# Kernel tuning notes

Hardware: AMD Instinct MI355X
Metric: run time of the kernel (lower is better)

## Reference

```python
import jax, jax.numpy as jnp
import numpy as np

NS = 100000   # served nodes
NI = 100000   # interfered nodes
E = 1000000   # edges per relation
D = 64        # 2 * Nt_num, Nt_num = 32
HM = 32       # message MLP hidden
HU = 16       # update MLP hidden


def _lin_init(key, fan_in, fan_out):
    s = 1.0 / np.sqrt(fan_in)
    kw, kb = jax.random.split(key)
    w = jax.random.uniform(kw, (fan_in, fan_out), jnp.float32, -s, s)
    b = jax.random.uniform(kb, (fan_out,), jnp.float32, -s, s)
    return w, b


def setup_inputs() -> dict:
    key = jax.random.key(0)
    ks = jax.random.split(key, 12)
    wm1, bm1 = _lin_init(ks[0], D, HM)
    wm2, bm2 = _lin_init(ks[1], HM, D)
    wu1, bu1 = _lin_init(ks[2], D, HU)
    wu2, bu2 = _lin_init(ks[3], HU, D)
    wo, bo = _lin_init(ks[4], D, D)
    edge_s2i = jnp.stack([
        jax.random.randint(ks[5], (E,), 0, NS),   # src in served
        jax.random.randint(ks[6], (E,), 0, NI),   # dst in interfered
    ]).astype(jnp.int64)
    edge_i2s = jnp.stack([
        jax.random.randint(ks[7], (E,), 0, NI),   # src in interfered
        jax.random.randint(ks[8], (E,), 0, NS),   # dst in served
    ]).astype(jnp.int64)
    return {
        "x_served": jax.random.normal(ks[9], (NS, D), jnp.float32),
        "x_interfered": jax.random.normal(ks[10], (NI, D), jnp.float32),
        "edge_s2i": edge_s2i,
        "edge_i2s": edge_i2s,
        "wm1": wm1, "bm1": bm1, "wm2": wm2, "bm2": bm2,
        "wu1": wu1, "bu1": bu1, "wu2": wu2, "bu2": bu2,
        "wo": wo, "bo": bo,
    }


def reference(x_served, x_interfered, edge_s2i, edge_i2s,
              wm1, bm1, wm2, bm2, wu1, bu1, wu2, bu2, wo, bo):
    def mlp_m(h):  # MLP([D, 32, D]): Lin+ReLU, Lin+ReLU
        return jax.nn.relu(jax.nn.relu(h @ wm1 + bm1) @ wm2 + bm2)

    def mlp_u(h):  # MLP([D, 16, D])
        return jax.nn.relu(jax.nn.relu(h @ wu1 + bu1) @ wu2 + bu2)

    def conv(x_src, edges, n_dst):
        # gather source node features per edge, per-edge message MLP
        msg = mlp_m(x_src[edges[0]])                    # [E, D]
        # scatter-sum into destination nodes
        agg = jax.ops.segment_sum(msg, edges[1], num_segments=n_dst)
        return mlp_u(agg)                               # [n_dst, D]

    xs, xi = x_served, x_interfered
    for _ in range(3):
        new_i = conv(xs, edge_s2i, NI)   # served -> interfered
        new_s = conv(xi, edge_i2s, NS)   # interfered -> served
        xs, xi = new_s, new_i
    # h2o on served: Lin + Tanh -> beamforming matrix
    return jnp.tanh(xs @ wo + bo)
```

## Files before the change

kernel.cpp:

```cpp
#include <hip/hip_runtime.h>
#include <hip/hip_fp16.h>
#include <math.h>

constexpr int D = 64;
constexpr int CAP = 48;
constexpr int RPB = 256;
constexpr int EPB = 4096;

typedef _Float16 half2_t __attribute__((ext_vector_type(2)));

__device__ inline float fdot2(unsigned a, unsigned b, float c){
    return __builtin_amdgcn_fdot2(__builtin_bit_cast(half2_t, a),
                                  __builtin_bit_cast(half2_t, b), c, false);
}

__device__ inline unsigned pack2(float lo, float hi){
    __half2 h = __floats2half2_rn(lo, hi);
    return *(unsigned*)&h;
}

__device__ inline void ld16u(const unsigned* base, unsigned* w){
    const uint4* p = (const uint4*)base;
    uint4 a = p[0], b = p[1], c = p[2], d = p[3];
    w[0]=a.x;  w[1]=a.y;  w[2]=a.z;  w[3]=a.w;
    w[4]=b.x;  w[5]=b.y;  w[6]=b.z;  w[7]=b.w;
    w[8]=c.x;  w[9]=c.y;  w[10]=c.z; w[11]=c.w;
    w[12]=d.x; w[13]=d.y; w[14]=d.z; w[15]=d.w;
}

__device__ inline void store_half8(__half* dst, const float* o){
    uint4 w;
    w.x = pack2(o[0], o[1]); w.y = pack2(o[2], o[3]);
    w.z = pack2(o[4], o[5]); w.w = pack2(o[6], o[7]);
    *((uint4*)dst) = w;
}

__device__ inline void load_half8(const __half* src, float* r){
    uint4 w = *((const uint4*)src);
    __half2* h = (__half2*)&w;
    float2 f0 = __half22float2(h[0]);
    float2 f1 = __half22float2(h[1]);
    float2 f2 = __half22float2(h[2]);
    float2 f3 = __half22float2(h[3]);
    r[0] = f0.x; r[1] = f0.y; r[2] = f1.x; r[3] = f1.y;
    r[4] = f2.x; r[5] = f2.y; r[6] = f3.x; r[7] = f3.y;
}


__global__ void __launch_bounds__(256) k_bucket_mlpm(
        const int* __restrict__ es2i, const int* __restrict__ ei2s, int E, int NI,
        int NBUK, int BSTRIDE,
        int* __restrict__ gcur, unsigned* __restrict__ buckets,
        const float* __restrict__ x,
        const float* __restrict__ wm1, const float* __restrict__ bm1,
        const float* __restrict__ wm2, const float* __restrict__ bm2,
        __half* __restrict__ y, int Nmlp, int nbEdge)
{
    __shared__ __align__(16) char smem[12544];
    int t = threadIdx.x;

    if ((int)blockIdx.x < nbEdge){
        int* hist = (int*)smem;
        int* base = (int*)(smem + 4096);
        int* offs = (int*)(smem + 8192);
        for (int i = t; i < NBUK; i += 256){ hist[i] = 0; offs[i] = 0; }
        __syncthreads();
        int e0 = blockIdx.x * EPB + t;
        int rr[16], ss[16];
        #pragma unroll
        for (int k = 0; k < 16; k++){
            int i = e0 + k*256;
            if (i < E){
                ss[k] = es2i[i];            rr[k] = es2i[E + i];
            } else if (i < 2*E){
                int j = i - E;
                ss[k] = ei2s[j];            rr[k] = NI + ei2s[E + j];
            } else rr[k] = -1;
        }
        #pragma unroll
        for (int k = 0; k < 16; k++)
            if (rr[k] >= 0) atomicAdd(&hist[rr[k] >> 8], 1);
        __syncthreads();
        for (int b = t; b < NBUK; b += 256){
            int h = hist[b];
            base[b] = h ? atomicAdd(&gcur[b], h) : 0;
        }
        __syncthreads();
        #pragma unroll
        for (int k = 0; k < 16; k++){
            if (rr[k] >= 0){
                int b = rr[k] >> 8;
                int p = base[b] + atomicAdd(&offs[b], 1);
                if (p < BSTRIDE)
                    buckets[(size_t)b*BSTRIDE + p] =
                        ((unsigned)(rr[k] & 255) << 24) | (unsigned)ss[k];
            }
        }
        return;
    }

    unsigned* w1p = (unsigned*)smem;
    unsigned* w2p = (unsigned*)(smem + 4096);
    float*    sb1 = (float*)(smem + 8192);
    float*    sb2 = (float*)(smem + 8320);
    for (int i = t; i < 1024; i += 256){ int kp=i>>5, j=i&31; w1p[i]=pack2(wm1[(2*kp)*32+j], wm1[(2*kp+1)*32+j]); }
    for (int i = t; i < 1024; i += 256){ int jp=i>>6, c=i&63; w2p[i]=pack2(wm2[(2*jp)*64+c], wm2[(2*jp+1)*64+c]); }
    if (t < 32) sb1[t] = bm1[t];
    if (t < 64) sb2[t] = bm2[t];
    __syncthreads();
    int n = ((int)blockIdx.x - nbEdge)*256 + t;
    if (n >= Nmlp) return;

    const float4* xp = (const float4*)(x + (size_t)n*D);
    unsigned xq[32];
    #pragma unroll
    for (int i = 0; i < 16; i++){
        float4 v = xp[i];
        xq[2*i]   = pack2(v.x, v.y);
        xq[2*i+1] = pack2(v.z, v.w);
    }
    float h[32];
    #pragma unroll
    for (int j = 0; j < 32; j++) h[j] = 0.f;
    #pragma unroll
    for (int kp = 0; kp < 32; kp++){
        unsigned xv = xq[kp];
        unsigned w[32];
        ld16u(&w1p[kp*32],      w);
        ld16u(&w1p[kp*32 + 16], w + 16);
        #pragma unroll
        for (int j = 0; j < 32; j++) h[j] = fdot2(xv, w[j], h[j]);
    }
    #pragma unroll
    for (int j = 0; j < 32; j++) h[j] = fmaxf(h[j] + sb1[j], 0.f);
    unsigned hh[16];
    #pragma unroll
    for (int jp = 0; jp < 16; jp++) hh[jp] = pack2(h[2*jp], h[2*jp+1]);

    __half* yrow = y + (size_t)n*D;
    #pragma unroll
    for (int c0 = 0; c0 < 64; c0 += 32){
        float o[32];
        #pragma unroll
        for (int c = 0; c < 32; c++) o[c] = sb2[c0 + c];
        #pragma unroll
        for (int jp = 0; jp < 16; jp++){
            unsigned hv = hh[jp];
            unsigned w[32];
            ld16u(&w2p[jp*64 + c0],      w);
            ld16u(&w2p[jp*64 + c0 + 16], w + 16);
            #pragma unroll
            for (int c = 0; c < 32; c++) o[c] = fdot2(hv, w[c], o[c]);
        }
        #pragma unroll
        for (int c = 0; c < 32; c++) o[c] = fmaxf(o[c], 0.f);
        store_half8(yrow + c0,      &o[0]);
        store_half8(yrow + c0 + 8,  &o[8]);
        store_half8(yrow + c0 + 16, &o[16]);
        store_half8(yrow + c0 + 24, &o[24]);
    }
}


__global__ void __launch_bounds__(512) k_scatter_lds(const int* __restrict__ gcur,
        const unsigned* __restrict__ buckets, int BSTRIDE, int NTOT,
        int* __restrict__ cnt, int* __restrict__ slots)
{
    __shared__ int lcnt[RPB];
    __shared__ int lslots[RPB*CAP];
    int t = threadIdx.x;
    int b = blockIdx.x;
    int r0 = b * RPB;
    int nrows = NTOT - r0; if (nrows > RPB) nrows = RPB;

    for (int i = t; i < RPB; i += 512) lcnt[i] = 0;
    __syncthreads();

    int n = gcur[b]; if (n > BSTRIDE) n = BSTRIDE;
    const unsigned* bp = buckets + (size_t)b*BSTRIDE;
    for (int k = t; k < n; k += 512){
        unsigned e = bp[k];
        int lr  = e >> 24;
        int src = e & 0xFFFFFF;
        int pos = atomicAdd(&lcnt[lr], 1);
        if (pos < CAP) lslots[lr*CAP + pos] = src;
    }
    __syncthreads();

    int4* gs = (int4*)(slots + (size_t)r0*CAP);
    const int4* ls = (const int4*)lslots;
    int n4 = nrows*CAP/4;
    for (int i = t; i < n4; i += 512) gs[i] = ls[i];
    for (int i = t; i < nrows; i += 512) cnt[r0 + i] = lcnt[i];
}


__global__ void __launch_bounds__(256) k_agg(const __half* __restrict__ M,
        const int* __restrict__ cnt, const int* __restrict__ slots,
        __half* __restrict__ agg, int N)
{
    int gid  = blockIdx.x*256 + threadIdx.x;
    int node = gid >> 6;
    if (node >= N) return;
    int lane = gid & 63;
    int sub  = lane >> 3;
    int fl   = lane & 7;
    int deg = cnt[node]; deg = deg < CAP ? deg : CAP;
    const int* row = slots + (size_t)node*CAP;
    float acc[8];
    #pragma unroll
    for (int i = 0; i < 8; i++) acc[i] = 0.f;
    for (int k = sub; k < deg; k += 8){
        int s = row[k];
        float v[8];
        load_half8(M + (size_t)s*D + fl*8, v);
        #pragma unroll
        for (int i = 0; i < 8; i++) acc[i] += v[i];
    }
    #pragma unroll
    for (int i = 0; i < 8; i++){
        acc[i] += __shfl_xor(acc[i], 8);
        acc[i] += __shfl_xor(acc[i], 16);
        acc[i] += __shfl_xor(acc[i], 32);
    }
    if (sub == 0) store_half8(agg + (size_t)node*D + fl*8, acc);
}


__global__ void __launch_bounds__(256) k_mlp_um(const __half* __restrict__ agg,
        const float* __restrict__ wu1, const float* __restrict__ bu1,
        const float* __restrict__ wu2, const float* __restrict__ bu2,
        const float* __restrict__ wm1, const float* __restrict__ bm1,
        const float* __restrict__ wm2, const float* __restrict__ bm2,
        __half* __restrict__ y, int N)
{
    __shared__ __align__(16) unsigned w1p[32*16];
    __shared__ __align__(16) unsigned w2p[8*64];
    __shared__ __align__(16) unsigned m1p[32*32];
    __shared__ __align__(16) unsigned m2p[16*64];
    __shared__ float sbu1[16], sbu2[64], sbm1[32], sbm2[64];
    int t = threadIdx.x;
    for (int i = t; i < 512;  i += 256){ int kp=i>>4, j=i&15; w1p[i]=pack2(wu1[(2*kp)*16+j], wu1[(2*kp+1)*16+j]); }
    for (int i = t; i < 512;  i += 256){ int jp=i>>6, c=i&63; w2p[i]=pack2(wu2[(2*jp)*64+c], wu2[(2*jp+1)*64+c]); }
    for (int i = t; i < 1024; i += 256){ int kp=i>>5, j=i&31; m1p[i]=pack2(wm1[(2*kp)*32+j], wm1[(2*kp+1)*32+j]); }
    for (int i = t; i < 1024; i += 256){ int kp=i>>6, c=i&63; m2p[i]=pack2(wm2[(2*kp)*64+c], wm2[(2*kp+1)*64+c]); }
    if (t < 16) sbu1[t] = bu1[t];
    if (t < 64) sbu2[t] = bu2[t];
    if (t < 32) sbm1[t] = bm1[t];
    if (t < 64) sbm2[t] = bm2[t];
    __syncthreads();
    int n = blockIdx.x*256 + t;
    if (n >= N) return;

    unsigned xq[32];
    {
        const uint4* p = (const uint4*)(agg + (size_t)n*D);
        #pragma unroll
        for (int i = 0; i < 8; i++){
            uint4 w = p[i];
            xq[4*i] = w.x; xq[4*i+1] = w.y; xq[4*i+2] = w.z; xq[4*i+3] = w.w;
        }
    }

    float h[16];
    #pragma unroll
    for (int j = 0; j < 16; j++) h[j] = 0.f;
    #pragma unroll
    for (int kp = 0; kp < 32; kp++){
        unsigned a = xq[kp];
        unsigned w[16];
        ld16u(&w1p[kp*16], w);
        #pragma unroll
        for (int j = 0; j < 16; j++) h[j] = fdot2(a, w[j], h[j]);
    }
    #pragma unroll
    for (int j = 0; j < 16; j++) h[j] = fmaxf(h[j] + sbu1[j], 0.f);
    unsigned hp[8];
    #pragma unroll
    for (int jp = 0; jp < 8; jp++) hp[jp] = pack2(h[2*jp], h[2*jp+1]);

    #pragma unroll
    for (int c0 = 0; c0 < 64; c0 += 32){
        float o[32];
        #pragma unroll
        for (int c = 0; c < 32; c++) o[c] = sbu2[c0 + c];
        #pragma unroll
        for (int jp = 0; jp < 8; jp++){
            unsigned a = hp[jp];
            unsigned w[32];
            ld16u(&w2p[jp*64 + c0],      w);
            ld16u(&w2p[jp*64 + c0 + 16], w + 16);
            #pragma unroll
            for (int c = 0; c < 32; c++) o[c] = fdot2(a, w[c], o[c]);
        }
        #pragma unroll
        for (int c = 0; c < 32; c += 2)
            xq[(c0 + c) >> 1] = pack2(fmaxf(o[c], 0.f), fmaxf(o[c+1], 0.f));
    }

    float hm[32];
    #pragma unroll
    for (int j = 0; j < 32; j++) hm[j] = 0.f;
    #pragma unroll
    for (int kp = 0; kp < 32; kp++){
        unsigned a = xq[kp];
        unsigned w[32];
        ld16u(&m1p[kp*32],      w);
        ld16u(&m1p[kp*32 + 16], w + 16);
        #pragma unroll
        for (int j = 0; j < 32; j++) hm[j] = fdot2(a, w[j], hm[j]);
    }
    #pragma unroll
    for (int j = 0; j < 32; j++) hm[j] = fmaxf(hm[j] + sbm1[j], 0.f);
    unsigned hq[16];
    #pragma unroll
    for (int jp = 0; jp < 16; jp++) hq[jp] = pack2(hm[2*jp], hm[2*jp+1]);

    __half* yrow = y + (size_t)n*D;
    #pragma unroll
    for (int c0 = 0; c0 < 64; c0 += 32){
        float o[32];
        #pragma unroll
        for (int c = 0; c < 32; c++) o[c] = sbm2[c0 + c];
        #pragma unroll
        for (int kp = 0; kp < 16; kp++){
            unsigned a = hq[kp];
            unsigned w[32];
            ld16u(&m2p[kp*64 + c0],      w);
            ld16u(&m2p[kp*64 + c0 + 16], w + 16);
            #pragma unroll
            for (int c = 0; c < 32; c++) o[c] = fdot2(a, w[c], o[c]);
        }
        #pragma unroll
        for (int c = 0; c < 32; c++) o[c] = fmaxf(o[c], 0.f);
        store_half8(yrow + c0,      &o[0]);
        store_half8(yrow + c0 + 8,  &o[8]);
        store_half8(yrow + c0 + 16, &o[16]);
        store_half8(yrow + c0 + 24, &o[24]);
    }
}


__device__ inline float fast_tanh(float x){
    float ax = fabsf(x);
    float e  = __expf(2.f*ax);
    float t  = 1.f - 2.f/(e + 1.f);
    return copysignf(t, x);
}

__global__ void __launch_bounds__(256) k_mlp_uo(const __half* __restrict__ agg,
        const float* __restrict__ wu1, const float* __restrict__ bu1,
        const float* __restrict__ wu2, const float* __restrict__ bu2,
        const float* __restrict__ wo,  const float* __restrict__ bo,
        float* __restrict__ out, int N)
{
    __shared__ __align__(16) unsigned w1p[32*16];
    __shared__ __align__(16) unsigned w2p[8*64];
    __shared__ __align__(16) unsigned wop[32*64];
    __shared__ float sbu1[16], sbu2[64], sbo[64];
    int t = threadIdx.x;
    for (int i = t; i < 512;  i += 256){ int kp=i>>4, j=i&15; w1p[i]=pack2(wu1[(2*kp)*16+j], wu1[(2*kp+1)*16+j]); }
    for (int i = t; i < 512;  i += 256){ int jp=i>>6, c=i&63; w2p[i]=pack2(wu2[(2*jp)*64+c], wu2[(2*jp+1)*64+c]); }
    for (int i = t; i < 2048; i += 256){ int kp=i>>6, c=i&63; wop[i]=pack2(wo[(2*kp)*64+c], wo[(2*kp+1)*64+c]); }
    if (t < 16) sbu1[t] = bu1[t];
    if (t < 64) sbu2[t] = bu2[t];
    if (t < 64) sbo[t]  = bo[t];
    __syncthreads();
    int n = blockIdx.x*256 + t;
    if (n >= N) return;

    unsigned xq[32];
    {
        const uint4* p = (const uint4*)(agg + (size_t)n*D);
        #pragma unroll
        for (int i = 0; i < 8; i++){
            uint4 w = p[i];
            xq[4*i] = w.x; xq[4*i+1] = w.y; xq[4*i+2] = w.z; xq[4*i+3] = w.w;
        }
    }

    float h[16];
    #pragma unroll
    for (int j = 0; j < 16; j++) h[j] = 0.f;
    #pragma unroll
    for (int kp = 0; kp < 32; kp++){
        unsigned a = xq[kp];
        unsigned w[16];
        ld16u(&w1p[kp*16], w);
        #pragma unroll
        for (int j = 0; j < 16; j++) h[j] = fdot2(a, w[j], h[j]);
    }
    #pragma unroll
    for (int j = 0; j < 16; j++) h[j] = fmaxf(h[j] + sbu1[j], 0.f);
    unsigned hp[8];
    #pragma unroll
    for (int jp = 0; jp < 8; jp++) hp[jp] = pack2(h[2*jp], h[2*jp+1]);

    #pragma unroll
    for (int c0 = 0; c0 < 64; c0 += 32){
        float o[32];
        #pragma unroll
        for (int c = 0; c < 32; c++) o[c] = sbu2[c0 + c];
        #pragma unroll
        for (int jp = 0; jp < 8; jp++){
            unsigned a = hp[jp];
            unsigned w[32];
            ld16u(&w2p[jp*64 + c0],      w);
            ld16u(&w2p[jp*64 + c0 + 16], w + 16);
            #pragma unroll
            for (int c = 0; c < 32; c++) o[c] = fdot2(a, w[c], o[c]);
        }
        #pragma unroll
        for (int c = 0; c < 32; c += 2)
            xq[(c0 + c) >> 1] = pack2(fmaxf(o[c], 0.f), fmaxf(o[c+1], 0.f));
    }

    float* orow = out + (size_t)n*D;
    #pragma unroll
    for (int c0 = 0; c0 < 64; c0 += 32){
        float o[32];
        #pragma unroll
        for (int c = 0; c < 32; c++) o[c] = sbo[c0 + c];
        #pragma unroll
        for (int kp = 0; kp < 32; kp++){
            unsigned a = xq[kp];
            unsigned w[32];
            ld16u(&wop[kp*64 + c0],      w);
            ld16u(&wop[kp*64 + c0 + 16], w + 16);
            #pragma unroll
            for (int c = 0; c < 32; c++) o[c] = fdot2(a, w[c], o[c]);
        }
        float4* op = (float4*)(orow + c0);
        #pragma unroll
        for (int i = 0; i < 8; i++){
            float4 v;
            v.x = fast_tanh(o[4*i]);
            v.y = fast_tanh(o[4*i+1]);
            v.z = fast_tanh(o[4*i+2]);
            v.w = fast_tanh(o[4*i+3]);
            op[i] = v;
        }
    }
}


extern "C" void kernel_launch(void* const* d_in, const int* in_sizes, int n_in,
                              void* d_out, int out_size, void* d_ws, size_t ws_size,
                              hipStream_t stream)
{
    const float* x_interfered = (const float*)d_in[1];
    const int*   e_s2i        = (const int*)d_in[2];
    const int*   e_i2s        = (const int*)d_in[3];
    const float* wm1 = (const float*)d_in[4];  const float* bm1 = (const float*)d_in[5];
    const float* wm2 = (const float*)d_in[6];  const float* bm2 = (const float*)d_in[7];
    const float* wu1 = (const float*)d_in[8];  const float* bu1 = (const float*)d_in[9];
    const float* wu2 = (const float*)d_in[10]; const float* bu2 = (const float*)d_in[11];
    const float* wo  = (const float*)d_in[12]; const float* bo  = (const float*)d_in[13];

    const int NS = in_sizes[0] / D;
    const int NI = in_sizes[1] / D;
    const int E  = in_sizes[2] / 2;
    const int NMAX = (NS > NI) ? NS : NI;
    const int NTOT = NI + NS;

    const int NBUK = ((NTOT - 1) >> 8) + 1;
    int avg = (2*E) / NBUK;
    const int BSTRIDE = ((2*avg) + 1023) & ~1023;

    char* p = (char*)d_ws;
    auto alloc = [&](size_t bytes) -> void* {
        void* r = (void*)p;
        p += (bytes + 255) & ~(size_t)255;
        return r;
    };
    __half*   M      = (__half*)alloc((size_t)NMAX*D*2);
    __half*   AGG    = (__half*)alloc((size_t)NMAX*D*2);
    int*      cnt    = (int*)alloc((size_t)NTOT*4);
    int*      gcur   = (int*)alloc((size_t)NBUK*4);
    int*      slots  = (int*)alloc((size_t)NTOT*CAP*4);
    unsigned* buckets= (unsigned*)alloc((size_t)NBUK*BSTRIDE*4);
    (void)ws_size; (void)n_in; (void)out_size;

    const int* cnt_i = cnt;
    const int* cnt_s = cnt + NI;
    const int* slots_i = slots;
    const int* slots_s = slots + (size_t)NI*CAP;

    hipMemsetAsync(gcur, 0, (size_t)NBUK*4, stream);

    const int nbEdge = (2*E + EPB - 1)/EPB;
    const int nbMlp  = (NI + 255)/256;
    k_bucket_mlpm<<<nbEdge + nbMlp, 256, 0, stream>>>(
        e_s2i, e_i2s, E, NI, NBUK, BSTRIDE, gcur, buckets,
        x_interfered, wm1, bm1, wm2, bm2, M, NI, nbEdge);
    k_scatter_lds<<<NBUK, 512, 0, stream>>>(gcur, buckets, BSTRIDE, NTOT, cnt, slots);

    k_agg<<<((size_t)NS*64 + 255)/256, 256, 0, stream>>>(M, cnt_s, slots_s, AGG, NS);
    k_mlp_um<<<(NS + 255)/256, 256, 0, stream>>>(AGG, wu1, bu1, wu2, bu2,
                                               wm1, bm1, wm2, bm2, M, NS);
    k_agg<<<((size_t)NI*64 + 255)/256, 256, 0, stream>>>(M, cnt_i, slots_i, AGG, NI);
    k_mlp_um<<<(NI + 255)/256, 256, 0, stream>>>(AGG, wu1, bu1, wu2, bu2,
                                               wm1, bm1, wm2, bm2, M, NI);
    k_agg<<<((size_t)NS*64 + 255)/256, 256, 0, stream>>>(M, cnt_s, slots_s, AGG, NS);
    k_mlp_uo<<<(NS + 255)/256, 256, 0, stream>>>(AGG, wu1, bu1, wu2, bu2,
                                               wo, bo, (float*)d_out, NS);
}
```

Before: 248.1 us.

## Process two nodes per thread in MLP kernels and halve edge-bucketing chunk

The node-MLP kernels now run 128 threads per block, and each thread handles two nodes. Every weight fragment read from shared memory is reused for both nodes, which cuts LDS traffic per FLOP, and output chunks shrink to 16 columns to limit register pressure. Separately, the edge-bucketing blocks each take 2048 edges instead of 4096. That doubles the block count for parallelism but also doubles the per-block histogram init and the global atomic traffic. The two-node register arrays may raise VGPR use and lower occupancy.

```diff
diff --git a/kernel.cpp b/kernel.cpp
--- a/kernel.cpp
+++ b/kernel.cpp
@@ -5,7 +5,7 @@
 constexpr int D = 64;
 constexpr int CAP = 48;
 constexpr int RPB = 256;
-constexpr int EPB = 4096;
+constexpr int EPB = 2048;
 
 typedef _Float16 half2_t __attribute__((ext_vector_type(2)));
 
@@ -66,9 +66,9 @@
         for (int i = t; i < NBUK; i += 256){ hist[i] = 0; offs[i] = 0; }
         __syncthreads();
         int e0 = blockIdx.x * EPB + t;
-        int rr[16], ss[16];
-        #pragma unroll
-        for (int k = 0; k < 16; k++){
+        int rr[8], ss[8];
+        #pragma unroll
+        for (int k = 0; k < 8; k++){
             int i = e0 + k*256;
             if (i < E){
                 ss[k] = es2i[i];            rr[k] = es2i[E + i];
@@ -78,7 +78,7 @@
             } else rr[k] = -1;
         }
         #pragma unroll
-        for (int k = 0; k < 16; k++)
+        for (int k = 0; k < 8; k++)
             if (rr[k] >= 0) atomicAdd(&hist[rr[k] >> 8], 1);
         __syncthreads();
         for (int b = t; b < NBUK; b += 256){
@@ -87,7 +87,7 @@
         }
         __syncthreads();
         #pragma unroll
-        for (int k = 0; k < 16; k++){
+        for (int k = 0; k < 8; k++){
             if (rr[k] >= 0){
                 int b = rr[k] >> 8;
                 int p = base[b] + atomicAdd(&offs[b], 1);
@@ -227,7 +227,7 @@
 }
 
 
-__global__ void __launch_bounds__(256) k_mlp_um(const __half* __restrict__ agg,
+__global__ void __launch_bounds__(128) k_mlp_um(const __half* __restrict__ agg,
         const float* __restrict__ wu1, const float* __restrict__ bu1,
         const float* __restrict__ wu2, const float* __restrict__ bu2,
         const float* __restrict__ wm1, const float* __restrict__ bm1,
@@ -240,103 +240,143 @@
     __shared__ __align__(16) unsigned m2p[16*64];
     __shared__ float sbu1[16], sbu2[64], sbm1[32], sbm2[64];
     int t = threadIdx.x;
-    for (int i = t; i < 512;  i += 256){ int kp=i>>4, j=i&15; w1p[i]=pack2(wu1[(2*kp)*16+j], wu1[(2*kp+1)*16+j]); }
-    for (int i = t; i < 512;  i += 256){ int jp=i>>6, c=i&63; w2p[i]=pack2(wu2[(2*jp)*64+c], wu2[(2*jp+1)*64+c]); }
-    for (int i = t; i < 1024; i += 256){ int kp=i>>5, j=i&31; m1p[i]=pack2(wm1[(2*kp)*32+j], wm1[(2*kp+1)*32+j]); }
-    for (int i = t; i < 1024; i += 256){ int kp=i>>6, c=i&63; m2p[i]=pack2(wm2[(2*kp)*64+c], wm2[(2*kp+1)*64+c]); }
+    for (int i = t; i < 512;  i += 128){ int kp=i>>4, j=i&15; w1p[i]=pack2(wu1[(2*kp)*16+j], wu1[(2*kp+1)*16+j]); }
+    for (int i = t; i < 512;  i += 128){ int jp=i>>6, c=i&63; w2p[i]=pack2(wu2[(2*jp)*64+c], wu2[(2*jp+1)*64+c]); }
+    for (int i = t; i < 1024; i += 128){ int kp=i>>5, j=i&31; m1p[i]=pack2(wm1[(2*kp)*32+j], wm1[(2*kp+1)*32+j]); }
+    for (int i = t; i < 1024; i += 128){ int kp=i>>6, c=i&63; m2p[i]=pack2(wm2[(2*kp)*64+c], wm2[(2*kp+1)*64+c]); }
     if (t < 16) sbu1[t] = bu1[t];
     if (t < 64) sbu2[t] = bu2[t];
     if (t < 32) sbm1[t] = bm1[t];
     if (t < 64) sbm2[t] = bm2[t];
     __syncthreads();
-    int n = blockIdx.x*256 + t;
-    if (n >= N) return;
-
-    unsigned xq[32];
+    int base = blockIdx.x*256;
+    int n0 = base + t;
+    int n1 = base + t + 128;
+    bool has0 = n0 < N;
+    bool has1 = n1 < N;
+    if (!has0) return;
+
+    unsigned xq0[32], xq1[32];
     {
-        const uint4* p = (const uint4*)(agg + (size_t)n*D);
+        const uint4* p = (const uint4*)(agg + (size_t)n0*D);
         #pragma unroll
         for (int i = 0; i < 8; i++){
             uint4 w = p[i];
-            xq[4*i] = w.x; xq[4*i+1] = w.y; xq[4*i+2] = w.z; xq[4*i+3] = w.w;
-        }
-    }
-
-    float h[16];
-    #pragma unroll
-    for (int j = 0; j < 16; j++) h[j] = 0.f;
+            xq0[4*i] = w.x; xq0[4*i+1] = w.y; xq0[4*i+2] = w.z; xq0[4*i+3] = w.w;
+        }
+    }
+    if (has1){
+        const uint4* p = (const uint4*)(agg + (size_t)n1*D);
+        #pragma unroll
+        for (int i = 0; i < 8; i++){
+            uint4 w = p[i];
+            xq1[4*i] = w.x; xq1[4*i+1] = w.y; xq1[4*i+2] = w.z; xq1[4*i+3] = w.w;
+        }
+    } else {
+        #pragma unroll
+        for (int i = 0; i < 32; i++) xq1[i] = 0u;
+    }
+
+    float h0[16], h1[16];
+    #pragma unroll
+    for (int j = 0; j < 16; j++){ h0[j] = 0.f; h1[j] = 0.f; }
     #pragma unroll
     for (int kp = 0; kp < 32; kp++){
-        unsigned a = xq[kp];
+        unsigned a0 = xq0[kp], a1 = xq1[kp];
         unsigned w[16];
         ld16u(&w1p[kp*16], w);
         #pragma unroll
-        for (int j = 0; j < 16; j++) h[j] = fdot2(a, w[j], h[j]);
-    }
-    #pragma unroll
-    for (int j = 0; j < 16; j++) h[j] = fmaxf(h[j] + sbu1[j], 0.f);
-    unsigned hp[8];
-    #pragma unroll
-    for (int jp = 0; jp < 8; jp++) hp[jp] = pack2(h[2*jp], h[2*jp+1]);
-
-    #pragma unroll
-    for (int c0 = 0; c0 < 64; c0 += 32){
-        float o[32];
-        #pragma unroll
-        for (int c = 0; c < 32; c++) o[c] = sbu2[c0 + c];
+        for (int j = 0; j < 16; j++){
+            h0[j] = fdot2(a0, w[j], h0[j]);
+            h1[j] = fdot2(a1, w[j], h1[j]);
+        }
+    }
+    unsigned hp0[8], hp1[8];
+    #pragma unroll
+    for (int jp = 0; jp < 8; jp++){
+        float a0 = fmaxf(h0[2*jp]   + sbu1[2*jp],   0.f);
+        float b0 = fmaxf(h0[2*jp+1] + sbu1[2*jp+1], 0.f);
+        float a1 = fmaxf(h1[2*jp]   + sbu1[2*jp],   0.f);
+        float b1 = fmaxf(h1[2*jp+1] + sbu1[2*jp+1], 0.f);
+        hp0[jp] = pack2(a0, b0);
+        hp1[jp] = pack2(a1, b1);
+    }
+
+    #pragma unroll
+    for (int c0 = 0; c0 < 64; c0 += 16){
+        float o0[16], o1[16];
+        #pragma unroll
+        for (int c = 0; c < 16; c++){ float bv = sbu2[c0 + c]; o0[c] = bv; o1[c] = bv; }
         #pragma unroll
         for (int jp = 0; jp < 8; jp++){
-            unsigned a = hp[jp];
-            unsigned w[32];
-            ld16u(&w2p[jp*64 + c0],      w);
-            ld16u(&w2p[jp*64 + c0 + 16], w + 16);
+            unsigned a0 = hp0[jp], a1 = hp1[jp];
+            unsigned w[16];
+            ld16u(&w2p[jp*64 + c0], w);
             #pragma unroll
-            for (int c = 0; c < 32; c++) o[c] = fdot2(a, w[c], o[c]);
-        }
-        #pragma unroll
-        for (int c = 0; c < 32; c += 2)
-            xq[(c0 + c) >> 1] = pack2(fmaxf(o[c], 0.f), fmaxf(o[c+1], 0.f));
-    }
-
-    float hm[32];
-    #pragma unroll
-    for (int j = 0; j < 32; j++) hm[j] = 0.f;
+            for (int c = 0; c < 16; c++){
+                o0[c] = fdot2(a0, w[c], o0[c]);
+                o1[c] = fdot2(a1, w[c], o1[c]);
+            }
+        }
+        #pragma unroll
+        for (int c = 0; c < 16; c += 2){
+            xq0[(c0 + c) >> 1] = pack2(fmaxf(o0[c], 0.f), fmaxf(o0[c+1], 0.f));
+            xq1[(c0 + c) >> 1] = pack2(fmaxf(o1[c], 0.f), fmaxf(o1[c+1], 0.f));
+        }
+    }
+
+    float hm0[32], hm1[32];
+    #pragma unroll
+    for (int j = 0; j < 32; j++){ hm0[j] = 0.f; hm1[j] = 0.f; }
     #pragma unroll
     for (int kp = 0; kp < 32; kp++){
-        unsigned a = xq[kp];
+        unsigned a0 = xq0[kp], a1 = xq1[kp];
         unsigned w[32];
         ld16u(&m1p[kp*32],      w);
         ld16u(&m1p[kp*32 + 16], w + 16);
         #pragma unroll
-        for (int j = 0; j < 32; j++) hm[j] = fdot2(a, w[j], hm[j]);
-    }
-    #pragma unroll
-    for (int j = 0; j < 32; j++) hm[j] = fmaxf(hm[j] + sbm1[j], 0.f);
-    unsigned hq[16];
-    #pragma unroll
-    for (int jp = 0; jp < 16; jp++) hq[jp] = pack2(hm[2*jp], hm[2*jp+1]);
-
-    __half* yrow = y + (size_t)n*D;
-    #pragma unroll
-    for (int c0 = 0; c0 < 64; c0 += 32){
-        float o[32];
-        #pragma unroll
-        for (int c = 0; c < 32; c++) o[c] = sbm2[c0 + c];
+        for (int j = 0; j < 32; j++){
+            hm0[j] = fdot2(a0, w[j], hm0[j]);
+            hm1[j] = fdot2(a1, w[j], hm1[j]);
+        }
+    }
+    unsigned hq0[16], hq1[16];
+    #pragma unroll
+    for (int jp = 0; jp < 16; jp++){
+        float a0 = fmaxf(hm0[2*jp]   + sbm1[2*jp],   0.f);
+        float b0 = fmaxf(hm0[2*jp+1] + sbm1[2*jp+1], 0.f);
+        float a1 = fmaxf(hm1[2*jp]   + sbm1[2*jp],   0.f);
+        float b1 = fmaxf(hm1[2*jp+1] + sbm1[2*jp+1], 0.f);
+        hq0[jp] = pack2(a0, b0);
+        hq1[jp] = pack2(a1, b1);
+    }
+
+    __half* yr0 = y + (size_t)n0*D;
+    __half* yr1 = y + (size_t)n1*D;
+    #pragma unroll
+    for (int c0 = 0; c0 < 64; c0 += 16){
+        float o0[16], o1[16];
+        #pragma unroll
+        for (int c = 0; c < 16; c++){ float bv = sbm2[c0 + c]; o0[c] = bv; o1[c] = bv; }
         #pragma unroll
         for (int kp = 0; kp < 16; kp++){
-            unsigned a = hq[kp];
-            unsigned w[32];
-            ld16u(&m2p[kp*64 + c0],      w);
-            ld16u(&m2p[kp*64 + c0 + 16], w + 16);
+            unsigned a0 = hq0[kp], a1 = hq1[kp];
+            unsigned w[16];
+            ld16u(&m2p[kp*64 + c0], w);
             #pragma unroll
-            for (int c = 0; c < 32; c++) o[c] = fdot2(a, w[c], o[c]);
-        }
-        #pragma unroll
-        for (int c = 0; c < 32; c++) o[c] = fmaxf(o[c], 0.f);
-        store_half8(yrow + c0,      &o[0]);
-        store_half8(yrow + c0 + 8,  &o[8]);
-        store_half8(yrow + c0 + 16, &o[16]);
-        store_half8(yrow + c0 + 24, &o[24]);
+            for (int c = 0; c < 16; c++){
+                o0[c] = fdot2(a0, w[c], o0[c]);
+                o1[c] = fdot2(a1, w[c], o1[c]);
+            }
+        }
+        #pragma unroll
+        for (int c = 0; c < 16; c++){ o0[c] = fmaxf(o0[c], 0.f); o1[c] = fmaxf(o1[c], 0.f); }
+        store_half8(yr0 + c0,     &o0[0]);
+        store_half8(yr0 + c0 + 8, &o0[8]);
+        if (has1){
+            store_half8(yr1 + c0,     &o1[0]);
+            store_half8(yr1 + c0 + 8, &o1[8]);
+        }
     }
 }
 
@@ -348,7 +388,7 @@
     return copysignf(t, x);
 }
 
-__global__ void __launch_bounds__(256) k_mlp_uo(const __half* __restrict__ agg,
+__global__ void __launch_bounds__(128) k_mlp_uo(const __half* __restrict__ agg,
         const float* __restrict__ wu1, const float* __restrict__ bu1,
         const float* __restrict__ wu2, const float* __restrict__ bu2,
         const float* __restrict__ wo,  const float* __restrict__ bo,
@@ -359,86 +399,128 @@
     __shared__ __align__(16) unsigned wop[32*64];
     __shared__ float sbu1[16], sbu2[64], sbo[64];
     int t = threadIdx.x;
-    for (int i = t; i < 512;  i += 256){ int kp=i>>4, j=i&15; w1p[i]=pack2(wu1[(2*kp)*16+j], wu1[(2*kp+1)*16+j]); }
-    for (int i = t; i < 512;  i += 256){ int jp=i>>6, c=i&63; w2p[i]=pack2(wu2[(2*jp)*64+c], wu2[(2*jp+1)*64+c]); }
-    for (int i = t; i < 2048; i += 256){ int kp=i>>6, c=i&63; wop[i]=pack2(wo[(2*kp)*64+c], wo[(2*kp+1)*64+c]); }
+    for (int i = t; i < 512;  i += 128){ int kp=i>>4, j=i&15; w1p[i]=pack2(wu1[(2*kp)*16+j], wu1[(2*kp+1)*16+j]); }
+    for (int i = t; i < 512;  i += 128){ int jp=i>>6, c=i&63; w2p[i]=pack2(wu2[(2*jp)*64+c], wu2[(2*jp+1)*64+c]); }
+    for (int i = t; i < 2048; i += 128){ int kp=i>>6, c=i&63; wop[i]=pack2(wo[(2*kp)*64+c], wo[(2*kp+1)*64+c]); }
     if (t < 16) sbu1[t] = bu1[t];
     if (t < 64) sbu2[t] = bu2[t];
     if (t < 64) sbo[t]  = bo[t];
     __syncthreads();
-    int n = blockIdx.x*256 + t;
-    if (n >= N) return;
-
-    unsigned xq[32];
+    int base = blockIdx.x*256;
+    int n0 = base + t;
+    int n1 = base + t + 128;
+    bool has0 = n0 < N;
+    bool has1 = n1 < N;
+    if (!has0) return;
+
+    unsigned xq0[32], xq1[32];
     {
-        const uint4* p = (const uint4*)(agg + (size_t)n*D);
+        const uint4* p = (const uint4*)(agg + (size_t)n0*D);
         #pragma unroll
         for (int i = 0; i < 8; i++){
             uint4 w = p[i];
-            xq[4*i] = w.x; xq[4*i+1] = w.y; xq[4*i+2] = w.z; xq[4*i+3] = w.w;
-        }
-    }
-
-    float h[16];
-    #pragma unroll
-    for (int j = 0; j < 16; j++) h[j] = 0.f;
+            xq0[4*i] = w.x; xq0[4*i+1] = w.y; xq0[4*i+2] = w.z; xq0[4*i+3] = w.w;
+        }
+    }
+    if (has1){
+        const uint4* p = (const uint4*)(agg + (size_t)n1*D);
+        #pragma unroll
+        for (int i = 0; i < 8; i++){
+            uint4 w = p[i];
+            xq1[4*i] = w.x; xq1[4*i+1] = w.y; xq1[4*i+2] = w.z; xq1[4*i+3] = w.w;
+        }
+    } else {
+        #pragma unroll
+        for (int i = 0; i < 32; i++) xq1[i] = 0u;
+    }
+
+    float h0[16], h1[16];
+    #pragma unroll
+    for (int j = 0; j < 16; j++){ h0[j] = 0.f; h1[j] = 0.f; }
     #pragma unroll
     for (int kp = 0; kp < 32; kp++){
-        unsigned a = xq[kp];
+        unsigned a0 = xq0[kp], a1 = xq1[kp];
         unsigned w[16];
         ld16u(&w1p[kp*16], w);
         #pragma unroll
-        for (int j = 0; j < 16; j++) h[j] = fdot2(a, w[j], h[j]);
-    }
-    #pragma unroll
-    for (int j = 0; j < 16; j++) h[j] = fmaxf(h[j] + sbu1[j], 0.f);
-    unsigned hp[8];
-    #pragma unroll
-    for (int jp = 0; jp < 8; jp++) hp[jp] = pack2(h[2*jp], h[2*jp+1]);
-
-    #pragma unroll
-    for (int c0 = 0; c0 < 64; c0 += 32){
-        float o[32];
-        #pragma unroll
-        for (int c = 0; c < 32; c++) o[c] = sbu2[c0 + c];
+        for (int j = 0; j < 16; j++){
+            h0[j] = fdot2(a0, w[j], h0[j]);
+            h1[j] = fdot2(a1, w[j], h1[j]);
+        }
+    }
+    unsigned hp0[8], hp1[8];
+    #pragma unroll
+    for (int jp = 0; jp < 8; jp++){
+        float a0 = fmaxf(h0[2*jp]   + sbu1[2*jp],   0.f);
+        float b0 = fmaxf(h0[2*jp+1] + sbu1[2*jp+1], 0.f);
+        float a1 = fmaxf(h1[2*jp]   + sbu1[2*jp],   0.f);
+        float b1 = fmaxf(h1[2*jp+1] + sbu1[2*jp+1], 0.f);
+        hp0[jp] = pack2(a0, b0);
+        hp1[jp] = pack2(a1, b1);
+    }
+
+    #pragma unroll
+    for (int c0 = 0; c0 < 64; c0 += 16){
+        float o0[16], o1[16];
+        #pragma unroll
+        for (int c = 0; c < 16; c++){ float bv = sbu2[c0 + c]; o0[c] = bv; o1[c] = bv; }
         #pragma unroll
         for (int jp = 0; jp < 8; jp++){
-            unsigned a = hp[jp];
-            unsigned w[32];
-            ld16u(&w2p[jp*64 + c0],      w);
-            ld16u(&w2p[jp*64 + c0 + 16], w + 16);
+            unsigned a0 = hp0[jp], a1 = hp1[jp];
+            unsigned w[16];
+            ld16u(&w2p[jp*64 + c0], w);
             #pragma unroll
-            for (int c = 0; c < 32; c++) o[c] = fdot2(a, w[c], o[c]);
-        }
-        #pragma unroll
-        for (int c = 0; c < 32; c += 2)
-            xq[(c0 + c) >> 1] = pack2(fmaxf(o[c], 0.f), fmaxf(o[c+1], 0.f));
-    }
-
-    float* orow = out + (size_t)n*D;
-    #pragma unroll
-    for (int c0 = 0; c0 < 64; c0 += 32){
-        float o[32];
-        #pragma unroll
-        for (int c = 0; c < 32; c++) o[c] = sbo[c0 + c];
+            for (int c = 0; c < 16; c++){
+                o0[c] = fdot2(a0, w[c], o0[c]);
+                o1[c] = fdot2(a1, w[c], o1[c]);
+            }
+        }
+        #pragma unroll
+        for (int c = 0; c < 16; c += 2){
+            xq0[(c0 + c) >> 1] = pack2(fmaxf(o0[c], 0.f), fmaxf(o0[c+1], 0.f));
+            xq1[(c0 + c) >> 1] = pack2(fmaxf(o1[c], 0.f), fmaxf(o1[c+1], 0.f));
+        }
+    }
+
+    float* or0 = out + (size_t)n0*D;
+    float* or1 = out + (size_t)n1*D;
+    #pragma unroll
+    for (int c0 = 0; c0 < 64; c0 += 16){
+        float o0[16], o1[16];
+        #pragma unroll
+        for (int c = 0; c < 16; c++){ float bv = sbo[c0 + c]; o0[c] = bv; o1[c] = bv; }
         #pragma unroll
         for (int kp = 0; kp < 32; kp++){
-            unsigned a = xq[kp];
-            unsigned w[32];
-            ld16u(&wop[kp*64 + c0],      w);
-            ld16u(&wop[kp*64 + c0 + 16], w + 16);
+            unsigned a0 = xq0[kp], a1 = xq1[kp];
+            unsigned w[16];
+            ld16u(&wop[kp*64 + c0], w);
             #pragma unroll
-            for (int c = 0; c < 32; c++) o[c] = fdot2(a, w[c], o[c]);
-        }
-        float4* op = (float4*)(orow + c0);
-        #pragma unroll
-        for (int i = 0; i < 8; i++){
+            for (int c = 0; c < 16; c++){
+                o0[c] = fdot2(a0, w[c], o0[c]);
+                o1[c] = fdot2(a1, w[c], o1[c]);
+            }
+        }
+        float4* op0 = (float4*)(or0 + c0);
+        #pragma unroll
+        for (int i = 0; i < 4; i++){
             float4 v;
-            v.x = fast_tanh(o[4*i]);
-            v.y = fast_tanh(o[4*i+1]);
-            v.z = fast_tanh(o[4*i+2]);
-            v.w = fast_tanh(o[4*i+3]);
-            op[i] = v;
+            v.x = fast_tanh(o0[4*i]);
+            v.y = fast_tanh(o0[4*i+1]);
+            v.z = fast_tanh(o0[4*i+2]);
+            v.w = fast_tanh(o0[4*i+3]);
+            op0[i] = v;
+        }
+        if (has1){
+            float4* op1 = (float4*)(or1 + c0);
+            #pragma unroll
+            for (int i = 0; i < 4; i++){
+                float4 v;
+                v.x = fast_tanh(o1[4*i]);
+                v.y = fast_tanh(o1[4*i+1]);
+                v.z = fast_tanh(o1[4*i+2]);
+                v.w = fast_tanh(o1[4*i+3]);
+                op1[i] = v;
+            }
         }
     }
 }
@@ -496,12 +578,12 @@
     k_scatter_lds<<<NBUK, 512, 0, stream>>>(gcur, buckets, BSTRIDE, NTOT, cnt, slots);
 
     k_agg<<<((size_t)NS*64 + 255)/256, 256, 0, stream>>>(M, cnt_s, slots_s, AGG, NS);
-    k_mlp_um<<<(NS + 255)/256, 256, 0, stream>>>(AGG, wu1, bu1, wu2, bu2,
+    k_mlp_um<<<(NS + 255)/256, 128, 0, stream>>>(AGG, wu1, bu1, wu2, bu2,
                                                wm1, bm1, wm2, bm2, M, NS);
     k_agg<<<((size_t)NI*64 + 255)/256, 256, 0, stream>>>(M, cnt_i, slots_i, AGG, NI);
-    k_mlp_um<<<(NI + 255)/256, 256, 0, stream>>>(AGG, wu1, bu1, wu2, bu2,
+    k_mlp_um<<<(NI + 255)/256, 128, 0, stream>>>(AGG, wu1, bu1, wu2, bu2,
                                                wm1, bm1, wm2, bm2, M, NI);
     k_agg<<<((size_t)NS*64 + 255)/256, 256, 0, stream>>>(M, cnt_s, slots_s, AGG, NS);
-    k_mlp_uo<<<(NS + 255)/256, 256, 0, stream>>>(AGG, wu1, bu1, wu2, bu2,
+    k_mlp_uo<<<(NS + 255)/256, 128, 0, stream>>>(AGG, wu1, bu1, wu2, bu2,
                                                wo, bo, (float*)d_out, NS);
 }
```

Measured after the change: 309.6 us. 1.25x slower.
